# Kernel tuning notes

Measured on AMD Instinct MI355X. Metric: run time of the kernel, lower is better.

Reference implementation:

```python
import jax, jax.numpy as jnp
import numpy as np
import math

K = 8  # n_prototypes
SQRT_2_OVER_PI = 0.7978845608028654  # sqrt(2/pi)
EPS = 1e-12  # torch F.normalize eps


def _gelu(x):
    # tanh-approx GELU, matching the module's _gelu
    return 0.5 * x * (1.0 + jnp.tanh(SQRT_2_OVER_PI * (x + 0.044715 * x * x * x)))


def _l2norm(x, axis=-1):
    n = jnp.linalg.norm(x, axis=axis, keepdims=True)
    return x / jnp.maximum(n, EPS)


def setup_inputs() -> dict:
    key = jax.random.key(0)
    k1, k2 = jax.random.split(key)
    B, T, D = 8, 2048, 2048
    x = jax.random.normal(k1, (B, T, D), dtype=jnp.float32)
    # prototype bank as it exists after initialization: unit-norm rows
    protos = _l2norm(jax.random.normal(k2, (K, D), dtype=jnp.float32))
    log_tau = jnp.asarray(math.log(2.0), dtype=jnp.float32)
    log_gamma = jnp.asarray(math.log(2.0), dtype=jnp.float32)
    log_blend = jnp.asarray(math.log(0.3 / 0.7), dtype=jnp.float32)
    return {"x": x, "protos": protos, "log_tau": log_tau,
            "log_gamma": log_gamma, "log_blend": log_blend}


def reference(x, protos, log_tau, log_gamma, log_blend):
    # steady-state (self._ready == True) forward path
    tau = jnp.exp(log_tau)
    gamma = jnp.exp(log_gamma)
    alpha = jax.nn.sigmoid(log_blend)

    out = _gelu(x)                                  # [B,T,D]
    out_norm = _l2norm(out)                         # [B,T,D]
    proto_norm = _l2norm(protos)                    # [K,D]
    sims = jnp.einsum('btd,kd->btk', out_norm, proto_norm)  # [B,T,K]
    soft_max_sim = (jax.nn.logsumexp(sims * tau, axis=-1) / tau
                    - jnp.log(jnp.float32(K)) / tau)         # [B,T]
    novelty = jnp.exp(-gamma * soft_max_sim)
    gate = 1.0 - alpha + alpha * novelty            # [B,T]
    return out * gate[..., None]
```

## Files before the change

### kernel.cpp

```cpp
#include <hip/hip_runtime.h>
#include <math.h>

#define DDIM 2048
#define KP 8
#define BLOCK 256

typedef float f4 __attribute__((ext_vector_type(4)));

#if __has_builtin(__builtin_amdgcn_fdot2_f32_bf16)
#define HAVE_DOT2 1
typedef __bf16 bf2 __attribute__((ext_vector_type(2)));
#else
#define HAVE_DOT2 0
#endif

#if __has_builtin(__builtin_amdgcn_update_dpp)
#define HAVE_DPP 1
#else
#define HAVE_DPP 0
#endif

__device__ __forceinline__ unsigned short f32_to_bf16_rne(float f) {
    unsigned u = __float_as_uint(f);
    unsigned r = u + 0x7FFFu + ((u >> 16) & 1u);
    return (unsigned short)(r >> 16);
}

__device__ __forceinline__ float gelu_f(float x) {
    float x2 = x * x;
    float inner = x * fmaf(0.044715f, x2, 1.0f);
    float e = __expf(-1.5957691216057308f * inner);
    return x * __builtin_amdgcn_rcpf(1.0f + e);
}

__device__ __forceinline__ float wave_reduce_add(float v) {
#pragma unroll
    for (int m = 32; m >= 1; m >>= 1) v += __shfl_xor(v, m, 64);
    return v;
}

#if HAVE_DPP
template <int CTRL>
__device__ __forceinline__ float dpp_add(float v) {
    int t = __builtin_amdgcn_update_dpp(0, __builtin_bit_cast(int, v),
                                        CTRL, 0xf, 0xf, true);
    return v + __builtin_bit_cast(float, t);
}
__device__ __forceinline__ float wave_sum_dpp_lane63(float v) {
    v = dpp_add<0x111>(v);
    v = dpp_add<0x112>(v);
    v = dpp_add<0x114>(v);
    v = dpp_add<0x118>(v);
    v = dpp_add<0x142>(v);
    v = dpp_add<0x143>(v);
    return v;
}
#endif

__global__ void proto_prep_kernel(const float* __restrict__ protos,
                                  unsigned short* __restrict__ pb,
                                  float* __restrict__ inv_pn) {
    const int k = blockIdx.x;
    const int tid = threadIdx.x;
    const float* p = protos + k * DDIM;
    float ss = 0.0f;
#pragma unroll
    for (int i = 0; i < 2; ++i) {
        int idx = tid + i * 256;
        f4 a = reinterpret_cast<const f4*>(p)[idx];
        ushort4 u;
        u.x = f32_to_bf16_rne(a.x); u.y = f32_to_bf16_rne(a.y);
        u.z = f32_to_bf16_rne(a.z); u.w = f32_to_bf16_rne(a.w);
        float q;
        q = __uint_as_float((unsigned)u.x << 16); ss += q * q;
        q = __uint_as_float((unsigned)u.y << 16); ss += q * q;
        q = __uint_as_float((unsigned)u.z << 16); ss += q * q;
        q = __uint_as_float((unsigned)u.w << 16); ss += q * q;
        *reinterpret_cast<ushort4*>(&pb[(size_t)k * DDIM + idx * 4]) = u;
    }
    ss = wave_reduce_add(ss);
    __shared__ float red[4];
    const int wave = tid >> 6, lane = tid & 63;
    if (lane == 0) red[wave] = ss;
    __syncthreads();
    if (tid == 0)
        inv_pn[k] = 1.0f / fmaxf(sqrtf(red[0] + red[1] + red[2] + red[3]), 1e-12f);
}

__global__ __launch_bounds__(BLOCK)
void fused_row_kernel(const float* __restrict__ x,
                      const unsigned short* __restrict__ pb,
                      const float* __restrict__ lt,
                      const float* __restrict__ lg,
                      const float* __restrict__ lb,
                      const float* __restrict__ inv_pn,
                      float* __restrict__ out, int nrows) {
    alignas(16) __shared__ float red[2][9][4];

    const int tid = threadIdx.x;
    const int lane = tid & 63;
    const int wave = tid >> 6;

    const float tau = __expf(lt[0]);
    const float gamma = __expf(lg[0]);
    const float alpha = 1.0f / (1.0f + __expf(-lb[0]));
    const float inv_tau = 1.0f / tau;
    const float logK_div_tau = logf(8.0f) * inv_tau;

    float ipn[KP];
#pragma unroll
    for (int k = 0; k < KP; ++k) ipn[k] = inv_pn[k];

    const uint2* pb2 = reinterpret_cast<const uint2*>(pb);

    int buf = 0;
    int row = blockIdx.x;
    f4 a, b;
    if (row < nrows) {
        const f4* xr = reinterpret_cast<const f4*>(x + (size_t)row * DDIM);
        a = xr[tid];
        b = xr[tid + 256];
    }

    for (; row < nrows; row += gridDim.x) {
        const int nxt = row + gridDim.x;
        f4 na, nb;
        if (nxt < nrows) {
            const f4* xn = reinterpret_cast<const f4*>(x + (size_t)nxt * DDIM);
            na = xn[tid];
            nb = xn[tid + 256];
        }

        f4 ga, gb;
        ga.x = gelu_f(a.x); ga.y = gelu_f(a.y);
        ga.z = gelu_f(a.z); ga.w = gelu_f(a.w);
        gb.x = gelu_f(b.x); gb.y = gelu_f(b.y);
        gb.z = gelu_f(b.z); gb.w = gelu_f(b.w);

        float vals[9];
        vals[8] = ga.x * ga.x + ga.y * ga.y + ga.z * ga.z + ga.w * ga.w
                + gb.x * gb.x + gb.y * gb.y + gb.z * gb.z + gb.w * gb.w;

#if HAVE_DOT2
        bf2 gp0, gp1, gp2, gp3;
        gp0.x = (__bf16)ga.x; gp0.y = (__bf16)ga.y;
        gp1.x = (__bf16)ga.z; gp1.y = (__bf16)ga.w;
        gp2.x = (__bf16)gb.x; gp2.y = (__bf16)gb.y;
        gp3.x = (__bf16)gb.z; gp3.y = (__bf16)gb.w;
#pragma unroll
        for (int k = 0; k < KP; ++k) {
            uint2 p0 = pb2[k * 512 + tid];
            uint2 p1 = pb2[k * 512 + 256 + tid];
            float t;
            t = __builtin_amdgcn_fdot2_f32_bf16(gp0, __builtin_bit_cast(bf2, p0.x), 0.0f, false);
            t = __builtin_amdgcn_fdot2_f32_bf16(gp1, __builtin_bit_cast(bf2, p0.y), t, false);
            t = __builtin_amdgcn_fdot2_f32_bf16(gp2, __builtin_bit_cast(bf2, p1.x), t, false);
            t = __builtin_amdgcn_fdot2_f32_bf16(gp3, __builtin_bit_cast(bf2, p1.y), t, false);
            vals[k] = t;
        }
#else
#pragma unroll
        for (int k = 0; k < KP; ++k) {
            uint2 p0 = pb2[k * 512 + tid];
            uint2 p1 = pb2[k * 512 + 256 + tid];
            float q0 = __uint_as_float(p0.x << 16);
            float q1 = __uint_as_float(p0.x & 0xFFFF0000u);
            float q2 = __uint_as_float(p0.y << 16);
            float q3 = __uint_as_float(p0.y & 0xFFFF0000u);
            float r0 = __uint_as_float(p1.x << 16);
            float r1 = __uint_as_float(p1.x & 0xFFFF0000u);
            float r2 = __uint_as_float(p1.y << 16);
            float r3 = __uint_as_float(p1.y & 0xFFFF0000u);
            float t;
            t = fmaf(q0, ga.x, q1 * ga.y);
            t = fmaf(q2, ga.z, t);
            t = fmaf(q3, ga.w, t);
            t = fmaf(r0, gb.x, t);
            t = fmaf(r1, gb.y, t);
            t = fmaf(r2, gb.z, t);
            t = fmaf(r3, gb.w, t);
            vals[k] = t;
        }
#endif

#if HAVE_DPP
#pragma unroll
        for (int v = 0; v < 9; ++v) vals[v] = wave_sum_dpp_lane63(vals[v]);
        if (lane == 63) {
#pragma unroll
            for (int v = 0; v < 9; ++v) red[buf][v][wave] = vals[v];
        }
#else
#pragma unroll
        for (int v = 0; v < 9; ++v) vals[v] = wave_reduce_add(vals[v]);
        if (lane == 0) {
#pragma unroll
            for (int v = 0; v < 9; ++v) red[buf][v][wave] = vals[v];
        }
#endif
        __syncthreads();

        float s[9];
#pragma unroll
        for (int v = 0; v < 9; ++v) {
            f4 r = *reinterpret_cast<const f4*>(red[buf][v]);
            s[v] = (r.x + r.y) + (r.z + r.w);
        }
        buf ^= 1;

        const float invn = 1.0f / fmaxf(sqrtf(s[8]), 1e-12f);
        float m = -1e30f;
        float z[KP];
#pragma unroll
        for (int k = 0; k < KP; ++k) {
            z[k] = s[k] * invn * ipn[k] * tau;
            m = fmaxf(m, z[k]);
        }
        float e = 0.0f;
#pragma unroll
        for (int k = 0; k < KP; ++k) e += __expf(z[k] - m);
        float lse = m + __logf(e);
        float sms = lse * inv_tau - logK_div_tau;
        float nov = __expf(-gamma * sms);
        const float gate = 1.0f - alpha + alpha * nov;

        f4* orow = reinterpret_cast<f4*>(out + (size_t)row * DDIM);
        f4 oa, ob;
        oa.x = ga.x * gate; oa.y = ga.y * gate;
        oa.z = ga.z * gate; oa.w = ga.w * gate;
        ob.x = gb.x * gate; ob.y = gb.y * gate;
        ob.z = gb.z * gate; ob.w = gb.w * gate;
        __builtin_nontemporal_store(oa, &orow[tid]);
        __builtin_nontemporal_store(ob, &orow[tid + 256]);

        a = na;
        b = nb;
    }
}

extern "C" void kernel_launch(void* const* d_in, const int* in_sizes, int n_in,
                              void* d_out, int out_size, void* d_ws, size_t ws_size,
                              hipStream_t stream) {
    const float* x = (const float*)d_in[0];
    const float* protos = (const float*)d_in[1];
    const float* lt = (const float*)d_in[2];
    const float* lg = (const float*)d_in[3];
    const float* lb = (const float*)d_in[4];
    float* out = (float*)d_out;

    float* inv_pn = (float*)d_ws;
    unsigned short* pb = (unsigned short*)((char*)d_ws + 256);

    const int nrows = in_sizes[0] / DDIM;

    proto_prep_kernel<<<KP, 256, 0, stream>>>(protos, pb, inv_pn);

    int blocks = nrows < 4096 ? nrows : 4096;
    fused_row_kernel<<<blocks, BLOCK, 0, stream>>>(x, pb, lt, lg, lb, inv_pn,
                                                   out, nrows);
}
```

Measured before the change: 52.17 us.

## Process two rows per block iteration, sharing prototype loads and one barrier

Each block iteration now handles two rows (r0 and r0+G), so each prototype load feeds two dot products and the two rows share one reduction barrier. The cross-iteration register prefetch of the next row is dropped; both rows are loaded at the top of the iteration. The grid is halved to at most 2048 blocks, and the logsumexp drops the max subtraction, which is safe only because the similarities are bounded by tau. Register pressure goes up and load/compute overlap now depends on occupancy rather than explicit prefetch.

```diff
diff --git a/kernel.cpp b/kernel.cpp
--- a/kernel.cpp
+++ b/kernel.cpp
@@ -95,7 +95,7 @@
                       const float* __restrict__ lb,
                       const float* __restrict__ inv_pn,
                       float* __restrict__ out, int nrows) {
-    alignas(16) __shared__ float red[2][9][4];
+    alignas(16) __shared__ float red[2][18][4];
 
     const int tid = threadIdx.x;
     const int lane = tid & 63;
@@ -112,129 +112,157 @@
     for (int k = 0; k < KP; ++k) ipn[k] = inv_pn[k];
 
     const uint2* pb2 = reinterpret_cast<const uint2*>(pb);
+    const int G = gridDim.x;
 
     int buf = 0;
-    int row = blockIdx.x;
-    f4 a, b;
-    if (row < nrows) {
-        const f4* xr = reinterpret_cast<const f4*>(x + (size_t)row * DDIM);
-        a = xr[tid];
-        b = xr[tid + 256];
-    }
-
-    for (; row < nrows; row += gridDim.x) {
-        const int nxt = row + gridDim.x;
-        f4 na, nb;
-        if (nxt < nrows) {
-            const f4* xn = reinterpret_cast<const f4*>(x + (size_t)nxt * DDIM);
-            na = xn[tid];
-            nb = xn[tid + 256];
-        }
-
-        f4 ga, gb;
-        ga.x = gelu_f(a.x); ga.y = gelu_f(a.y);
-        ga.z = gelu_f(a.z); ga.w = gelu_f(a.w);
-        gb.x = gelu_f(b.x); gb.y = gelu_f(b.y);
-        gb.z = gelu_f(b.z); gb.w = gelu_f(b.w);
-
-        float vals[9];
-        vals[8] = ga.x * ga.x + ga.y * ga.y + ga.z * ga.z + ga.w * ga.w
-                + gb.x * gb.x + gb.y * gb.y + gb.z * gb.z + gb.w * gb.w;
+    for (int r0 = blockIdx.x; r0 < nrows; r0 += 2 * G) {
+        const int r1 = r0 + G;
+        const bool has1 = r1 < nrows;
+
+        const f4* xr0 = reinterpret_cast<const f4*>(x + (size_t)r0 * DDIM);
+        f4 a0 = xr0[tid];
+        f4 b0 = xr0[tid + 256];
+        f4 a1, b1;
+        if (has1) {
+            const f4* xr1 = reinterpret_cast<const f4*>(x + (size_t)r1 * DDIM);
+            a1 = xr1[tid];
+            b1 = xr1[tid + 256];
+        } else {
+            a1 = a0; b1 = b0;
+        }
+
+        f4 g0a, g0b, g1a, g1b;
+        g0a.x = gelu_f(a0.x); g0a.y = gelu_f(a0.y);
+        g0a.z = gelu_f(a0.z); g0a.w = gelu_f(a0.w);
+        g0b.x = gelu_f(b0.x); g0b.y = gelu_f(b0.y);
+        g0b.z = gelu_f(b0.z); g0b.w = gelu_f(b0.w);
+        g1a.x = gelu_f(a1.x); g1a.y = gelu_f(a1.y);
+        g1a.z = gelu_f(a1.z); g1a.w = gelu_f(a1.w);
+        g1b.x = gelu_f(b1.x); g1b.y = gelu_f(b1.y);
+        g1b.z = gelu_f(b1.z); g1b.w = gelu_f(b1.w);
+
+        float vals[18];
+        vals[8] = g0a.x * g0a.x + g0a.y * g0a.y + g0a.z * g0a.z + g0a.w * g0a.w
+                + g0b.x * g0b.x + g0b.y * g0b.y + g0b.z * g0b.z + g0b.w * g0b.w;
+        vals[17] = g1a.x * g1a.x + g1a.y * g1a.y + g1a.z * g1a.z + g1a.w * g1a.w
+                 + g1b.x * g1b.x + g1b.y * g1b.y + g1b.z * g1b.z + g1b.w * g1b.w;
 
 #if HAVE_DOT2
-        bf2 gp0, gp1, gp2, gp3;
-        gp0.x = (__bf16)ga.x; gp0.y = (__bf16)ga.y;
-        gp1.x = (__bf16)ga.z; gp1.y = (__bf16)ga.w;
-        gp2.x = (__bf16)gb.x; gp2.y = (__bf16)gb.y;
-        gp3.x = (__bf16)gb.z; gp3.y = (__bf16)gb.w;
+        bf2 p0a, p0b, p0c, p0d, p1a, p1b, p1c, p1d;
+        p0a.x = (__bf16)g0a.x; p0a.y = (__bf16)g0a.y;
+        p0b.x = (__bf16)g0a.z; p0b.y = (__bf16)g0a.w;
+        p0c.x = (__bf16)g0b.x; p0c.y = (__bf16)g0b.y;
+        p0d.x = (__bf16)g0b.z; p0d.y = (__bf16)g0b.w;
+        p1a.x = (__bf16)g1a.x; p1a.y = (__bf16)g1a.y;
+        p1b.x = (__bf16)g1a.z; p1b.y = (__bf16)g1a.w;
+        p1c.x = (__bf16)g1b.x; p1c.y = (__bf16)g1b.y;
+        p1d.x = (__bf16)g1b.z; p1d.y = (__bf16)g1b.w;
 #pragma unroll
         for (int k = 0; k < KP; ++k) {
-            uint2 p0 = pb2[k * 512 + tid];
-            uint2 p1 = pb2[k * 512 + 256 + tid];
-            float t;
-            t = __builtin_amdgcn_fdot2_f32_bf16(gp0, __builtin_bit_cast(bf2, p0.x), 0.0f, false);
-            t = __builtin_amdgcn_fdot2_f32_bf16(gp1, __builtin_bit_cast(bf2, p0.y), t, false);
-            t = __builtin_amdgcn_fdot2_f32_bf16(gp2, __builtin_bit_cast(bf2, p1.x), t, false);
-            t = __builtin_amdgcn_fdot2_f32_bf16(gp3, __builtin_bit_cast(bf2, p1.y), t, false);
-            vals[k] = t;
+            uint2 q0 = pb2[k * 512 + tid];
+            uint2 q1 = pb2[k * 512 + 256 + tid];
+            float t0, t1;
+            t0 = __builtin_amdgcn_fdot2_f32_bf16(p0a, __builtin_bit_cast(bf2, q0.x), 0.0f, false);
+            t1 = __builtin_amdgcn_fdot2_f32_bf16(p1a, __builtin_bit_cast(bf2, q0.x), 0.0f, false);
+            t0 = __builtin_amdgcn_fdot2_f32_bf16(p0b, __builtin_bit_cast(bf2, q0.y), t0, false);
+            t1 = __builtin_amdgcn_fdot2_f32_bf16(p1b, __builtin_bit_cast(bf2, q0.y), t1, false);
+            t0 = __builtin_amdgcn_fdot2_f32_bf16(p0c, __builtin_bit_cast(bf2, q1.x), t0, false);
+            t1 = __builtin_amdgcn_fdot2_f32_bf16(p1c, __builtin_bit_cast(bf2, q1.x), t1, false);
+            t0 = __builtin_amdgcn_fdot2_f32_bf16(p0d, __builtin_bit_cast(bf2, q1.y), t0, false);
+            t1 = __builtin_amdgcn_fdot2_f32_bf16(p1d, __builtin_bit_cast(bf2, q1.y), t1, false);
+            vals[k] = t0;
+            vals[9 + k] = t1;
         }
 #else
 #pragma unroll
         for (int k = 0; k < KP; ++k) {
-            uint2 p0 = pb2[k * 512 + tid];
-            uint2 p1 = pb2[k * 512 + 256 + tid];
-            float q0 = __uint_as_float(p0.x << 16);
-            float q1 = __uint_as_float(p0.x & 0xFFFF0000u);
-            float q2 = __uint_as_float(p0.y << 16);
-            float q3 = __uint_as_float(p0.y & 0xFFFF0000u);
-            float r0 = __uint_as_float(p1.x << 16);
-            float r1 = __uint_as_float(p1.x & 0xFFFF0000u);
-            float r2 = __uint_as_float(p1.y << 16);
-            float r3 = __uint_as_float(p1.y & 0xFFFF0000u);
-            float t;
-            t = fmaf(q0, ga.x, q1 * ga.y);
-            t = fmaf(q2, ga.z, t);
-            t = fmaf(q3, ga.w, t);
-            t = fmaf(r0, gb.x, t);
-            t = fmaf(r1, gb.y, t);
-            t = fmaf(r2, gb.z, t);
-            t = fmaf(r3, gb.w, t);
-            vals[k] = t;
+            uint2 q0 = pb2[k * 512 + tid];
+            uint2 q1 = pb2[k * 512 + 256 + tid];
+            float c0 = __uint_as_float(q0.x << 16);
+            float c1 = __uint_as_float(q0.x & 0xFFFF0000u);
+            float c2 = __uint_as_float(q0.y << 16);
+            float c3 = __uint_as_float(q0.y & 0xFFFF0000u);
+            float c4 = __uint_as_float(q1.x << 16);
+            float c5 = __uint_as_float(q1.x & 0xFFFF0000u);
+            float c6 = __uint_as_float(q1.y << 16);
+            float c7 = __uint_as_float(q1.y & 0xFFFF0000u);
+            float t0, t1;
+            t0 = fmaf(c0, g0a.x, c1 * g0a.y);
+            t1 = fmaf(c0, g1a.x, c1 * g1a.y);
+            t0 = fmaf(c2, g0a.z, t0); t0 = fmaf(c3, g0a.w, t0);
+            t1 = fmaf(c2, g1a.z, t1); t1 = fmaf(c3, g1a.w, t1);
+            t0 = fmaf(c4, g0b.x, t0); t0 = fmaf(c5, g0b.y, t0);
+            t1 = fmaf(c4, g1b.x, t1); t1 = fmaf(c5, g1b.y, t1);
+            t0 = fmaf(c6, g0b.z, t0); t0 = fmaf(c7, g0b.w, t0);
+            t1 = fmaf(c6, g1b.z, t1); t1 = fmaf(c7, g1b.w, t1);
+            vals[k] = t0;
+            vals[9 + k] = t1;
         }
 #endif
 
 #if HAVE_DPP
 #pragma unroll
-        for (int v = 0; v < 9; ++v) vals[v] = wave_sum_dpp_lane63(vals[v]);
+        for (int v = 0; v < 18; ++v) vals[v] = wave_sum_dpp_lane63(vals[v]);
         if (lane == 63) {
 #pragma unroll
-            for (int v = 0; v < 9; ++v) red[buf][v][wave] = vals[v];
-        }
-#else
-#pragma unroll
-        for (int v = 0; v < 9; ++v) vals[v] = wave_reduce_add(vals[v]);
+            for (int v = 0; v < 18; ++v) red[buf][v][wave] = vals[v];
+        }
+#else
+#pragma unroll
+        for (int v = 0; v < 18; ++v) vals[v] = wave_reduce_add(vals[v]);
         if (lane == 0) {
 #pragma unroll
-            for (int v = 0; v < 9; ++v) red[buf][v][wave] = vals[v];
+            for (int v = 0; v < 18; ++v) red[buf][v][wave] = vals[v];
         }
 #endif
         __syncthreads();
 
-        float s[9];
-#pragma unroll
-        for (int v = 0; v < 9; ++v) {
+        float s[18];
+#pragma unroll
+        for (int v = 0; v < 18; ++v) {
             f4 r = *reinterpret_cast<const f4*>(red[buf][v]);
             s[v] = (r.x + r.y) + (r.z + r.w);
         }
         buf ^= 1;
 
-        const float invn = 1.0f / fmaxf(sqrtf(s[8]), 1e-12f);
-        float m = -1e30f;
-        float z[KP];
-#pragma unroll
-        for (int k = 0; k < KP; ++k) {
-            z[k] = s[k] * invn * ipn[k] * tau;
-            m = fmaxf(m, z[k]);
-        }
-        float e = 0.0f;
-#pragma unroll
-        for (int k = 0; k < KP; ++k) e += __expf(z[k] - m);
-        float lse = m + __logf(e);
-        float sms = lse * inv_tau - logK_div_tau;
-        float nov = __expf(-gamma * sms);
-        const float gate = 1.0f - alpha + alpha * nov;
-
-        f4* orow = reinterpret_cast<f4*>(out + (size_t)row * DDIM);
-        f4 oa, ob;
-        oa.x = ga.x * gate; oa.y = ga.y * gate;
-        oa.z = ga.z * gate; oa.w = ga.w * gate;
-        ob.x = gb.x * gate; ob.y = gb.y * gate;
-        ob.z = gb.z * gate; ob.w = gb.w * gate;
-        __builtin_nontemporal_store(oa, &orow[tid]);
-        __builtin_nontemporal_store(ob, &orow[tid + 256]);
-
-        a = na;
-        b = nb;
+        float gate0, gate1;
+        {
+            const float invn = 1.0f / fmaxf(sqrtf(s[8]), 1e-12f);
+            float e = 0.0f;
+#pragma unroll
+            for (int k = 0; k < KP; ++k)
+                e += __expf(s[k] * invn * ipn[k] * tau);
+            float sms = __logf(e) * inv_tau - logK_div_tau;
+            gate0 = 1.0f - alpha + alpha * __expf(-gamma * sms);
+        }
+        {
+            const float invn = 1.0f / fmaxf(sqrtf(s[17]), 1e-12f);
+            float e = 0.0f;
+#pragma unroll
+            for (int k = 0; k < KP; ++k)
+                e += __expf(s[9 + k] * invn * ipn[k] * tau);
+            float sms = __logf(e) * inv_tau - logK_div_tau;
+            gate1 = 1.0f - alpha + alpha * __expf(-gamma * sms);
+        }
+
+        f4* o0 = reinterpret_cast<f4*>(out + (size_t)r0 * DDIM);
+        f4 w0, w1;
+        w0.x = g0a.x * gate0; w0.y = g0a.y * gate0;
+        w0.z = g0a.z * gate0; w0.w = g0a.w * gate0;
+        w1.x = g0b.x * gate0; w1.y = g0b.y * gate0;
+        w1.z = g0b.z * gate0; w1.w = g0b.w * gate0;
+        __builtin_nontemporal_store(w0, &o0[tid]);
+        __builtin_nontemporal_store(w1, &o0[tid + 256]);
+        if (has1) {
+            f4* o1 = reinterpret_cast<f4*>(out + (size_t)r1 * DDIM);
+            f4 w2, w3;
+            w2.x = g1a.x * gate1; w2.y = g1a.y * gate1;
+            w2.z = g1a.z * gate1; w2.w = g1a.w * gate1;
+            w3.x = g1b.x * gate1; w3.y = g1b.y * gate1;
+            w3.z = g1b.z * gate1; w3.w = g1b.w * gate1;
+            __builtin_nontemporal_store(w2, &o1[tid]);
+            __builtin_nontemporal_store(w3, &o1[tid + 256]);
+        }
     }
 }
 
@@ -255,7 +283,8 @@
 
     proto_prep_kernel<<<KP, 256, 0, stream>>>(protos, pb, inv_pn);
 
-    int blocks = nrows < 4096 ? nrows : 4096;
+    int blocks = 2048;
+    if (blocks > (nrows + 1) / 2) blocks = (nrows + 1) / 2;
     fused_row_kernel<<<blocks, BLOCK, 0, stream>>>(x, pb, lt, lg, lb, inv_pn,
                                                    out, nrows);
 }
```

Measured after the change: 55.22 us. +5.9%, slower.
